# Optimization experiments

Measured on AMD Instinct MI355X. Metric: run time of the kernel, lower is better.

Reference implementation:

```python
import jax, jax.numpy as jnp
import numpy as np

N_USERS = 50000
N_ITEMS = 50000
N_NODES = N_USERS + N_ITEMS
N_EDGES = 1600000
D_IN = 128
D_OUT = 128


def setup_inputs() -> dict:
    key = jax.random.key(0)
    k1, k2, k3, k4, k5, k6 = jax.random.split(key, 6)
    u_f = jax.random.normal(k1, (N_USERS, D_IN), dtype=jnp.float32)
    v_f = jax.random.normal(k2, (N_ITEMS, D_IN), dtype=jnp.float32)
    adj_rows = jax.random.randint(k3, (N_EDGES,), 0, N_NODES, dtype=jnp.int32)
    adj_cols = jax.random.randint(k4, (N_EDGES,), 0, N_NODES, dtype=jnp.int32)
    adj_vals = jax.random.uniform(k5, (N_EDGES,), dtype=jnp.float32)
    # xavier_uniform init for weight [in_feats, out_feats]
    bound = float(np.sqrt(6.0 / (D_IN + D_OUT)))
    weight = jax.random.uniform(k6, (D_IN, D_OUT), dtype=jnp.float32,
                                minval=-bound, maxval=bound)
    return {"u_f": u_f, "v_f": v_f, "adj_rows": adj_rows,
            "adj_cols": adj_cols, "adj_vals": adj_vals, "weight": weight}


def reference(u_f, v_f, adj_rows, adj_cols, adj_vals, weight):
    # node_f = cat([u_f, v_f]) @ W          -- dense transform
    node_f = jnp.concatenate([u_f, v_f], axis=0)          # [N, D_in]
    node_f = node_f @ weight                               # [N, D_out]
    # sparse adjacency matmul: out[r] = sum_e vals[e] * node_f[cols[e]]
    msgs = adj_vals[:, None] * node_f[adj_cols]            # [E, D_out]
    out = jax.ops.segment_sum(msgs, adj_rows, num_segments=N_NODES)
    # activation (relu)
    return jax.nn.relu(out)
```

## Files before the change

### kernel.cpp

```cpp
#include <hip/hip_runtime.h>
#include <hip/hip_bf16.h>
#include <hip/hip_fp16.h>

#define N_USERS 50000
#define N_NODES 100000
#define N_EDGES 1600000
#define DIM 128
#define CAP 64

#define GEMM_BLOCKS 512
#define FILL_BLOCKS (N_EDGES / 256)
#define FUSED_GRID (GEMM_BLOCKS + FILL_BLOCKS)

typedef __attribute__((ext_vector_type(8))) _Float16 half8;
typedef __attribute__((ext_vector_type(4))) _Float16 half4;
typedef __attribute__((ext_vector_type(4))) float f32x4;

__global__ void zero_counts_kernel(int* __restrict__ counts) {
    int i = blockIdx.x * blockDim.x + threadIdx.x;
    if (i < N_NODES / 4) ((int4*)counts)[i] = (int4){0, 0, 0, 0};
}

__device__ __forceinline__ void gemm_body(
        const float* __restrict__ u_f, const float* __restrict__ v_f,
        const float* __restrict__ W, _Float16* __restrict__ node_f,
        _Float16* wfrag, int blockId, int nBlocks) {
    const int tid = threadIdx.x;

    for (int f = tid * 64, end = tid * 64 + 64; f < end; ++f) {
        const int ts   = f >> 9;
        const int rem  = f & 511;
        const int ln   = rem >> 3;
        const int j    = rem & 7;
        const int t    = ts >> 2;
        const int s    = ts & 3;
        const int krow = s * 32 + (ln >> 4) * 8 + j;
        const int col  = t * 16 + (ln & 15);
        wfrag[f] = (_Float16)W[krow * DIM + col];
    }
    __syncthreads();

    const int lane = tid & 63;
    const int wave = tid >> 6;
    const int m    = lane & 15;
    const int quad = lane >> 4;
    const int n_wtiles = N_NODES / 16;

    for (int wt = blockId * 4 + wave; wt < n_wtiles; wt += nBlocks * 4) {
        const int row = wt * 16 + m;
        const float* src = (row < N_USERS) ? u_f + (size_t)row * DIM
                                           : v_f + (size_t)(row - N_USERS) * DIM;
        f32x4 acc[8];
        #pragma unroll
        for (int t = 0; t < 8; ++t) acc[t] = (f32x4){0.f, 0.f, 0.f, 0.f};

        #pragma unroll
        for (int s = 0; s < 4; ++s) {
            const float* ap = src + s * 32 + quad * 8;
            const float4 a0 = *(const float4*)ap;
            const float4 a1 = *(const float4*)(ap + 4);
            half8 af;
            af[0] = (_Float16)a0.x; af[1] = (_Float16)a0.y;
            af[2] = (_Float16)a0.z; af[3] = (_Float16)a0.w;
            af[4] = (_Float16)a1.x; af[5] = (_Float16)a1.y;
            af[6] = (_Float16)a1.z; af[7] = (_Float16)a1.w;
            #pragma unroll
            for (int t = 0; t < 8; ++t) {
                const half8 wf = *(const half8*)&wfrag[((t * 4 + s) * 64 + lane) * 8];
                acc[t] = __builtin_amdgcn_mfma_f32_16x16x32_f16(af, wf, acc[t], 0, 0, 0);
            }
        }

        const int base = wt * 16;
        #pragma unroll
        for (int t = 0; t < 8; ++t) {
            #pragma unroll
            for (int r = 0; r < 4; ++r) {
                const int orow = base + quad * 4 + r;
                node_f[(size_t)orow * DIM + t * 16 + m] = (_Float16)acc[t][r];
            }
        }
    }
}

__global__ __launch_bounds__(256) void fused_gemm_fill_kernel(
        const float* __restrict__ u_f, const float* __restrict__ v_f,
        const float* __restrict__ W, _Float16* __restrict__ node_f,
        const int* __restrict__ rows, const int* __restrict__ cols,
        const float* __restrict__ vals,
        int* __restrict__ counts, long long* __restrict__ buckets) {
    __shared__ _Float16 wfrag[32 * 64 * 8];
    if (blockIdx.x < GEMM_BLOCKS) {
        gemm_body(u_f, v_f, W, node_f, wfrag, blockIdx.x, GEMM_BLOCKS);
        return;
    }
    const int e = (blockIdx.x - GEMM_BLOCKS) * 256 + threadIdx.x;
    const int r = rows[e];
    const int slot = atomicAdd(&counts[r], 1);
    if (slot < CAP) {
        const long long packed =
            ((long long)__float_as_int(vals[e]) << 32) | (unsigned)cols[e];
        buckets[(size_t)r * CAP + slot] = packed;
    }
}

__global__ __launch_bounds__(256) void gemm_mfma_kernel(
        const float* __restrict__ u_f, const float* __restrict__ v_f,
        const float* __restrict__ W, _Float16* __restrict__ node_f) {
    __shared__ _Float16 wfrag[32 * 64 * 8];
    gemm_body(u_f, v_f, W, node_f, wfrag, blockIdx.x, gridDim.x);
}

__global__ __launch_bounds__(256) void gather_kernel(
        const _Float16* __restrict__ node_f, const int* __restrict__ counts,
        const long long* __restrict__ buckets, float* __restrict__ out) {
    const int row  = (blockIdx.x * blockDim.x + threadIdx.x) >> 6;
    const int lane = threadIdx.x & 63;
    if (row >= N_NODES) return;
    const int pid = lane >> 5;
    const int cl  = lane & 31;

    int cnt = counts[row];
    if (cnt > CAP) cnt = CAP;

    int   col = 0;
    float val = 0.f;
    if (lane < cnt) {
        const long long p = buckets[(size_t)row * CAP + lane];
        col = (int)(unsigned)p;
        val = __int_as_float((int)(p >> 32));
    }

    f32x4 acc = {0.f, 0.f, 0.f, 0.f};
    int j = 0;
    for (; j + 8 <= cnt; j += 8) {
        int c[4]; float v[4]; half4 h[4];
        #pragma unroll
        for (int p = 0; p < 4; ++p) {
            c[p] = __shfl(col, j + 2 * p + pid, 64);
            v[p] = __shfl(val, j + 2 * p + pid, 64);
        }
        #pragma unroll
        for (int p = 0; p < 4; ++p)
            h[p] = *(const half4*)&node_f[(size_t)c[p] * DIM + cl * 4];
        #pragma unroll
        for (int p = 0; p < 4; ++p) {
            acc[0] += v[p] * (float)h[p][0];
            acc[1] += v[p] * (float)h[p][1];
            acc[2] += v[p] * (float)h[p][2];
            acc[3] += v[p] * (float)h[p][3];
        }
    }
    for (; j + 2 <= cnt; j += 2) {
        const int   c = __shfl(col, j + pid, 64);
        const float v = __shfl(val, j + pid, 64);
        const half4 h = *(const half4*)&node_f[(size_t)c * DIM + cl * 4];
        acc[0] += v * (float)h[0];
        acc[1] += v * (float)h[1];
        acc[2] += v * (float)h[2];
        acc[3] += v * (float)h[3];
    }
    if (j < cnt) {
        const int   c = __shfl(col, j, 64);
        const float vv = __shfl(val, j, 64);
        const float v = pid ? 0.f : vv;
        const half4 h = *(const half4*)&node_f[(size_t)c * DIM + cl * 4];
        acc[0] += v * (float)h[0];
        acc[1] += v * (float)h[1];
        acc[2] += v * (float)h[2];
        acc[3] += v * (float)h[3];
    }

    #pragma unroll
    for (int i = 0; i < 4; ++i) acc[i] += __shfl_xor(acc[i], 32, 64);

    if (pid == 0) {
        f32x4 r;
        r[0] = acc[0] > 0.f ? acc[0] : 0.f;
        r[1] = acc[1] > 0.f ? acc[1] : 0.f;
        r[2] = acc[2] > 0.f ? acc[2] : 0.f;
        r[3] = acc[3] > 0.f ? acc[3] : 0.f;
        __builtin_nontemporal_store(r, (f32x4*)&out[(size_t)row * DIM + cl * 4]);
    }
}

__global__ void zero_out_kernel(float* __restrict__ out) {
    int i = blockIdx.x * blockDim.x + threadIdx.x;
    int idx = i * 4;
    if (idx < N_NODES * DIM) {
        float4 z = {0.f, 0.f, 0.f, 0.f};
        *(float4*)&out[idx] = z;
    }
}

__global__ void scatter_kernel(const _Float16* __restrict__ node_f,
                               const int* __restrict__ rows, const int* __restrict__ cols,
                               const float* __restrict__ vals, float* __restrict__ out) {
    int t = blockIdx.x * blockDim.x + threadIdx.x;
    int e = t >> 5;
    int part = t & 31;
    if (e >= N_EDGES) return;
    int r = rows[e], c = cols[e];
    float v = vals[e];
    const __half2 h0 = *(const __half2*)&node_f[(size_t)c * DIM + part * 4];
    const __half2 h1 = *(const __half2*)&node_f[(size_t)c * DIM + part * 4 + 2];
    const float2 f0 = __half22float2(h0);
    const float2 f1 = __half22float2(h1);
    float* dst = &out[(size_t)r * DIM + part * 4];
    unsafeAtomicAdd(dst + 0, v * f0.x);
    unsafeAtomicAdd(dst + 1, v * f0.y);
    unsafeAtomicAdd(dst + 2, v * f1.x);
    unsafeAtomicAdd(dst + 3, v * f1.y);
}

__global__ void relu_kernel(float* __restrict__ out) {
    int i = blockIdx.x * blockDim.x + threadIdx.x;
    int idx = i * 4;
    if (idx < N_NODES * DIM) {
        float4 v = *(float4*)&out[idx];
        v.x = v.x > 0.f ? v.x : 0.f;
        v.y = v.y > 0.f ? v.y : 0.f;
        v.z = v.z > 0.f ? v.z : 0.f;
        v.w = v.w > 0.f ? v.w : 0.f;
        *(float4*)&out[idx] = v;
    }
}

extern "C" void kernel_launch(void* const* d_in, const int* in_sizes, int n_in,
                              void* d_out, int out_size, void* d_ws, size_t ws_size,
                              hipStream_t stream) {
    const float* u_f  = (const float*)d_in[0];
    const float* v_f  = (const float*)d_in[1];
    const int*   rows = (const int*)d_in[2];
    const int*   cols = (const int*)d_in[3];
    const float* vals = (const float*)d_in[4];
    const float* W    = (const float*)d_in[5];
    float* out = (float*)d_out;

    char* ws = (char*)d_ws;
    const size_t nodef_bytes  = (size_t)N_NODES * DIM * 2;
    const size_t counts_bytes = (size_t)N_NODES * 4;
    const size_t bucket_bytes = (size_t)N_NODES * CAP * 8;

    _Float16* node_f = (_Float16*)ws;
    int* counts = (int*)(ws + nodef_bytes);
    long long* buckets = (long long*)(ws + nodef_bytes + counts_bytes);

    if (ws_size >= nodef_bytes + counts_bytes + bucket_bytes) {
        zero_counts_kernel<<<(N_NODES / 4 + 255) / 256, 256, 0, stream>>>(counts);
        fused_gemm_fill_kernel<<<FUSED_GRID, 256, 0, stream>>>(
            u_f, v_f, W, node_f, rows, cols, vals, counts, buckets);
        gather_kernel<<<(N_NODES * 64 + 255) / 256, 256, 0, stream>>>(
            node_f, counts, buckets, out);
    } else {
        gemm_mfma_kernel<<<512, 256, 0, stream>>>(u_f, v_f, W, node_f);
        zero_out_kernel<<<(N_NODES * DIM / 4 + 255) / 256, 256, 0, stream>>>(out);
        scatter_kernel<<<((size_t)N_EDGES * 32 + 255) / 256, 256, 0, stream>>>(
            node_f, rows, cols, vals, out);
        relu_kernel<<<(N_NODES * DIM / 4 + 255) / 256, 256, 0, stream>>>(out);
    }
}
```

Measured before the change: 265.9 us.

## Pre-swizzle weights once in global memory and split GEMM tiles into half-width jobs

The W fp32-to-fp16 swizzle now runs once in a prep kernel that also zeroes the counts, instead of every GEMM block rebuilding it in shared memory. The GEMM reads the swizzled fragments straight from global memory (L2-resident), so it needs no LDS and no __syncthreads. Each wave job now covers half of the output columns, with 4 accumulators instead of 8, and the GEMM block count doubles with a launch-bounds occupancy hint. The cost is that each A row is loaded twice (once per column half), and weight fragments come from global or L2 instead of LDS.

```diff
diff --git a/kernel.cpp b/kernel.cpp
--- a/kernel.cpp
+++ b/kernel.cpp
@@ -8,7 +8,7 @@
 #define DIM 128
 #define CAP 64
 
-#define GEMM_BLOCKS 512
+#define GEMM_BLOCKS 1024
 #define FILL_BLOCKS (N_EDGES / 256)
 #define FUSED_GRID (GEMM_BLOCKS + FILL_BLOCKS)
 
@@ -16,43 +16,43 @@
 typedef __attribute__((ext_vector_type(4))) _Float16 half4;
 typedef __attribute__((ext_vector_type(4))) float f32x4;
 
-__global__ void zero_counts_kernel(int* __restrict__ counts) {
-    int i = blockIdx.x * blockDim.x + threadIdx.x;
-    if (i < N_NODES / 4) ((int4*)counts)[i] = (int4){0, 0, 0, 0};
+__global__ __launch_bounds__(256) void prep_kernel(
+        const float* __restrict__ W, int* __restrict__ counts,
+        _Float16* __restrict__ wswz, int do_counts) {
+    const int i = blockIdx.x * blockDim.x + threadIdx.x;
+    if (do_counts && i < N_NODES / 4) ((int4*)counts)[i] = (int4){0, 0, 0, 0};
+    if (i < DIM * DIM) {
+        const int j  = i & 7;
+        const int ln = (i >> 3) & 63;
+        const int ts = i >> 9;
+        const int t  = ts >> 2;
+        const int s  = ts & 3;
+        const int krow = s * 32 + (ln >> 4) * 8 + j;
+        const int col  = t * 16 + (ln & 15);
+        wswz[i] = (_Float16)W[krow * DIM + col];
+    }
 }
 
 __device__ __forceinline__ void gemm_body(
         const float* __restrict__ u_f, const float* __restrict__ v_f,
-        const float* __restrict__ W, _Float16* __restrict__ node_f,
-        _Float16* wfrag, int blockId, int nBlocks) {
-    const int tid = threadIdx.x;
-
-    for (int f = tid * 64, end = tid * 64 + 64; f < end; ++f) {
-        const int ts   = f >> 9;
-        const int rem  = f & 511;
-        const int ln   = rem >> 3;
-        const int j    = rem & 7;
-        const int t    = ts >> 2;
-        const int s    = ts & 3;
-        const int krow = s * 32 + (ln >> 4) * 8 + j;
-        const int col  = t * 16 + (ln & 15);
-        wfrag[f] = (_Float16)W[krow * DIM + col];
-    }
-    __syncthreads();
-
+        const _Float16* __restrict__ wswz, _Float16* __restrict__ node_f,
+        int blockId, int nBlocks) {
+    const int tid  = threadIdx.x;
     const int lane = tid & 63;
     const int wave = tid >> 6;
     const int m    = lane & 15;
     const int quad = lane >> 4;
-    const int n_wtiles = N_NODES / 16;
-
-    for (int wt = blockId * 4 + wave; wt < n_wtiles; wt += nBlocks * 4) {
+    const int n_jobs = (N_NODES / 16) * 2;
+
+    for (int w = blockId * 4 + wave; w < n_jobs; w += nBlocks * 4) {
+        const int wt = w >> 1;
+        const int h  = w & 1;
         const int row = wt * 16 + m;
         const float* src = (row < N_USERS) ? u_f + (size_t)row * DIM
                                            : v_f + (size_t)(row - N_USERS) * DIM;
-        f32x4 acc[8];
-        #pragma unroll
-        for (int t = 0; t < 8; ++t) acc[t] = (f32x4){0.f, 0.f, 0.f, 0.f};
+        f32x4 acc[4];
+        #pragma unroll
+        for (int t = 0; t < 4; ++t) acc[t] = (f32x4){0.f, 0.f, 0.f, 0.f};
 
         #pragma unroll
         for (int s = 0; s < 4; ++s) {
@@ -65,33 +65,33 @@
             af[4] = (_Float16)a1.x; af[5] = (_Float16)a1.y;
             af[6] = (_Float16)a1.z; af[7] = (_Float16)a1.w;
             #pragma unroll
-            for (int t = 0; t < 8; ++t) {
-                const half8 wf = *(const half8*)&wfrag[((t * 4 + s) * 64 + lane) * 8];
+            for (int t = 0; t < 4; ++t) {
+                const int tt = h * 4 + t;
+                const half8 wf = *(const half8*)&wswz[((tt * 4 + s) * 64 + lane) * 8];
                 acc[t] = __builtin_amdgcn_mfma_f32_16x16x32_f16(af, wf, acc[t], 0, 0, 0);
             }
         }
 
         const int base = wt * 16;
         #pragma unroll
-        for (int t = 0; t < 8; ++t) {
+        for (int t = 0; t < 4; ++t) {
             #pragma unroll
             for (int r = 0; r < 4; ++r) {
                 const int orow = base + quad * 4 + r;
-                node_f[(size_t)orow * DIM + t * 16 + m] = (_Float16)acc[t][r];
+                node_f[(size_t)orow * DIM + (h * 4 + t) * 16 + m] = (_Float16)acc[t][r];
             }
         }
     }
 }
 
-__global__ __launch_bounds__(256) void fused_gemm_fill_kernel(
+__global__ __launch_bounds__(256, 8) void fused_gemm_fill_kernel(
         const float* __restrict__ u_f, const float* __restrict__ v_f,
-        const float* __restrict__ W, _Float16* __restrict__ node_f,
+        const _Float16* __restrict__ wswz, _Float16* __restrict__ node_f,
         const int* __restrict__ rows, const int* __restrict__ cols,
         const float* __restrict__ vals,
         int* __restrict__ counts, long long* __restrict__ buckets) {
-    __shared__ _Float16 wfrag[32 * 64 * 8];
     if (blockIdx.x < GEMM_BLOCKS) {
-        gemm_body(u_f, v_f, W, node_f, wfrag, blockIdx.x, GEMM_BLOCKS);
+        gemm_body(u_f, v_f, wswz, node_f, blockIdx.x, GEMM_BLOCKS);
         return;
     }
     const int e = (blockIdx.x - GEMM_BLOCKS) * 256 + threadIdx.x;
@@ -104,11 +104,10 @@
     }
 }
 
-__global__ __launch_bounds__(256) void gemm_mfma_kernel(
+__global__ __launch_bounds__(256, 8) void gemm_mfma_kernel(
         const float* __restrict__ u_f, const float* __restrict__ v_f,
-        const float* __restrict__ W, _Float16* __restrict__ node_f) {
-    __shared__ _Float16 wfrag[32 * 64 * 8];
-    gemm_body(u_f, v_f, W, node_f, wfrag, blockIdx.x, gridDim.x);
+        const _Float16* __restrict__ wswz, _Float16* __restrict__ node_f) {
+    gemm_body(u_f, v_f, wswz, node_f, blockIdx.x, gridDim.x);
 }
 
 __global__ __launch_bounds__(256) void gather_kernel(
@@ -241,19 +240,23 @@
     const size_t nodef_bytes  = (size_t)N_NODES * DIM * 2;
     const size_t counts_bytes = (size_t)N_NODES * 4;
     const size_t bucket_bytes = (size_t)N_NODES * CAP * 8;
+    const size_t wswz_bytes   = (size_t)DIM * DIM * 2;
 
     _Float16* node_f = (_Float16*)ws;
     int* counts = (int*)(ws + nodef_bytes);
     long long* buckets = (long long*)(ws + nodef_bytes + counts_bytes);
-
-    if (ws_size >= nodef_bytes + counts_bytes + bucket_bytes) {
-        zero_counts_kernel<<<(N_NODES / 4 + 255) / 256, 256, 0, stream>>>(counts);
+    _Float16* wswz = (_Float16*)(ws + nodef_bytes + counts_bytes + bucket_bytes);
+
+    if (ws_size >= nodef_bytes + counts_bytes + bucket_bytes + wswz_bytes) {
+        prep_kernel<<<(N_NODES / 4 + 255) / 256, 256, 0, stream>>>(W, counts, wswz, 1);
         fused_gemm_fill_kernel<<<FUSED_GRID, 256, 0, stream>>>(
-            u_f, v_f, W, node_f, rows, cols, vals, counts, buckets);
+            u_f, v_f, wswz, node_f, rows, cols, vals, counts, buckets);
         gather_kernel<<<(N_NODES * 64 + 255) / 256, 256, 0, stream>>>(
             node_f, counts, buckets, out);
     } else {
-        gemm_mfma_kernel<<<512, 256, 0, stream>>>(u_f, v_f, W, node_f);
+        _Float16* wswz_fb = (_Float16*)(ws + nodef_bytes);
+        prep_kernel<<<(DIM * DIM + 255) / 256, 256, 0, stream>>>(W, nullptr, wswz_fb, 0);
+        gemm_mfma_kernel<<<1024, 256, 0, stream>>>(u_f, v_f, wswz_fb, node_f);
         zero_out_kernel<<<(N_NODES * DIM / 4 + 255) / 256, 256, 0, stream>>>(out);
         scatter_kernel<<<((size_t)N_EDGES * 32 + 255) / 256, 256, 0, stream>>>(
             node_f, rows, cols, vals, out);
```

Result: slower. 295.7 us (+11.2%).
